# Kernel tuning notes

Hardware: AMD Instinct MI355X
Metric: run time of the kernel (lower is better)

Reference implementation:

```python
import jax, jax.numpy as jnp
import numpy as np

D_MODEL = 1024
N_HEADS = 16
CHUNK_LEN = 50
MEM_LEN = 16
TOTAL_PROB = 20000
TOTAL_SKILL = 1000
B = 64
L = 2000
EPS = 1e-5


def _layernorm(x, g, b):
    mu = jnp.mean(x, axis=-1, keepdims=True)
    var = jnp.var(x, axis=-1, keepdims=True)
    return (x - mu) * jax.lax.rsqrt(var + EPS) * g + b


def setup_inputs() -> dict:
    key = jax.random.key(0)
    ks = jax.random.split(key, 20)
    s = 0.02
    D = D_MODEL
    emb_problem = (jax.random.normal(ks[0], (TOTAL_PROB, D), jnp.float32) * s).at[0].set(0.0)  # padding_idx=0
    emb_skill = (jax.random.normal(ks[1], (TOTAL_SKILL, D), jnp.float32) * s).at[0].set(0.0)
    mem_init = jax.random.normal(ks[2], (1, MEM_LEN, D), jnp.float32) * s
    pos_emb = jax.random.normal(ks[3], (MEM_LEN + CHUNK_LEN, D), jnp.float32) * s
    w_qkv = jax.random.normal(ks[4], (3 * D, D), jnp.float32) * s
    b_qkv = jnp.zeros((3 * D,), jnp.float32)
    w_out = jax.random.normal(ks[5], (D, D), jnp.float32) * s
    b_out = jnp.zeros((D,), jnp.float32)
    w1 = jax.random.normal(ks[6], (4 * D, D), jnp.float32) * s
    b1 = jnp.zeros((4 * D,), jnp.float32)
    w2 = jax.random.normal(ks[7], (D, 4 * D), jnp.float32) * s
    b2 = jnp.zeros((D,), jnp.float32)
    g_attn = jnp.ones((D,), jnp.float32)
    be_attn = jnp.zeros((D,), jnp.float32)
    g_ffn = jnp.ones((D,), jnp.float32)
    be_ffn = jnp.zeros((D,), jnp.float32)
    w_gate = jax.random.normal(ks[8], (D, D), jnp.float32) * s
    b_gate = jnp.zeros((D,), jnp.float32)
    in_prob = jax.random.randint(ks[9], (B, L), 0, TOTAL_PROB, dtype=jnp.int64 if jax.config.jax_enable_x64 else jnp.int32)
    in_skill = jax.random.randint(ks[10], (B, L), 0, TOTAL_SKILL, dtype=jnp.int64 if jax.config.jax_enable_x64 else jnp.int32)
    return dict(in_prob=in_prob, in_skill=in_skill, emb_problem=emb_problem, emb_skill=emb_skill,
                mem_init=mem_init, pos_emb=pos_emb, w_qkv=w_qkv, b_qkv=b_qkv, w_out=w_out, b_out=b_out,
                w1=w1, b1=b1, w2=w2, b2=b2, g_attn=g_attn, be_attn=be_attn, g_ffn=g_ffn, be_ffn=be_ffn,
                w_gate=w_gate, b_gate=b_gate)


def _mha(z, w_qkv, b_qkv, w_out, b_out, mask):
    # z: [B, T, D]; mask: [T, T] bool, True = disallowed (torch attn_mask semantics)
    Bz, T, D = z.shape
    dh = D // N_HEADS
    qkv = z @ w_qkv.T + b_qkv  # [B, T, 3D]
    q, k, v = jnp.split(qkv, 3, axis=-1)
    def heads(x):
        return x.reshape(Bz, T, N_HEADS, dh).transpose(0, 2, 1, 3)  # [B, H, T, dh]
    q, k, v = heads(q), heads(k), heads(v)
    scores = jnp.einsum('bhqd,bhkd->bhqk', q, k) / jnp.sqrt(jnp.float32(dh))
    scores = jnp.where(mask[None, None], jnp.float32(-1e9), scores)
    a = jax.nn.softmax(scores, axis=-1)
    o = jnp.einsum('bhqk,bhkd->bhqd', a, v)  # [B, H, T, dh]
    o = o.transpose(0, 2, 1, 3).reshape(Bz, T, D)
    return o @ w_out.T + b_out


def reference(in_prob, in_skill, emb_problem, emb_skill, mem_init, pos_emb,
              w_qkv, b_qkv, w_out, b_out, w1, b1, w2, b2,
              g_attn, be_attn, g_ffn, be_ffn, w_gate, b_gate):
    Bx, Lx = in_prob.shape
    D = emb_problem.shape[1]
    x = emb_problem[in_prob] + emb_skill[in_skill]  # [B, L, D]
    n_chunks = Lx // CHUNK_LEN
    T = MEM_LEN + CHUNK_LEN
    # block mask: memory fully visible, chunk part strictly causal
    causal = jnp.triu(jnp.ones((CHUNK_LEN, CHUNK_LEN), bool), k=1)
    mask = jnp.zeros((T, T), bool).at[MEM_LEN:, MEM_LEN:].set(causal)
    pos = pos_emb[:T][None]  # [1, T, D]
    chunks = x.reshape(Bx, n_chunks, CHUNK_LEN, D).transpose(1, 0, 2, 3)  # [K, B, Lc, D]
    mem0 = jnp.broadcast_to(mem_init, (Bx, MEM_LEN, D))

    def step(mem, xs):
        chunk, kidx = xs
        z = jnp.concatenate([mem, chunk], axis=1) + pos  # [B, T, D]
        z = z + _mha(_layernorm(z, g_attn, be_attn), w_qkv, b_qkv, w_out, b_out, mask)
        h = _layernorm(z, g_ffn, be_ffn)
        z = z + (jax.nn.relu(h @ w1.T + b1) @ w2.T + b2)
        mem_cand = z[:, :MEM_LEN]
        h_k = z[:, MEM_LEN:]
        g = jax.nn.sigmoid(mem_cand @ w_gate.T + b_gate)
        mem_gated = g * mem_cand + (1.0 - g) * mem
        mem_new = jnp.where(kidx == 0, mem_cand, mem_gated)  # first chunk: no gate
        return mem_new, h_k

    mem_final, hs = jax.lax.scan(step, mem0, (chunks, jnp.arange(n_chunks)))
    enc_out = hs.transpose(1, 0, 2, 3).reshape(Bx, Lx, D)
    return enc_out, mem_final
```

## Files before the change

kernel.cpp:

```cpp
#include <hip/hip_runtime.h>
#include <hip/hip_bf16.h>

#define D_MODEL 1024
#define N_HEADS 16
#define DH 64
#define CHUNK_LEN 50
#define MEM_LEN 16
#define TT 66
#define BB 64
#define LL 2000
#define NCHUNK 40
#define MTOK (BB*TT)

typedef _Float16 half8_t __attribute__((ext_vector_type(8)));
typedef __attribute__((ext_vector_type(4))) float f32x4;

typedef __attribute__((address_space(1))) const void GVoid;
typedef __attribute__((address_space(3))) void LVoid;

__device__ __forceinline__ void gload16(const void* g, void* l) {
  __builtin_amdgcn_global_load_lds((GVoid*)g, (LVoid*)l, 16, 0, 0);
}

__global__ __launch_bounds__(256) void f2h_kernel(const float* __restrict__ in,
                                                  _Float16* __restrict__ out, int n) {
  int i = (blockIdx.x * 256 + threadIdx.x) * 4;
  if (i < n) {
    float4 v = *(const float4*)(in + i);
    out[i+0] = (_Float16)v.x;
    out[i+1] = (_Float16)v.y;
    out[i+2] = (_Float16)v.z;
    out[i+3] = (_Float16)v.w;
  }
}

__global__ __launch_bounds__(256) void build_z_ln(
    const int* __restrict__ in_prob, const int* __restrict__ in_skill,
    const float* __restrict__ emb_p, const float* __restrict__ emb_s,
    const float* __restrict__ mem_src, int mem_bstride,
    const float* __restrict__ pos,
    const float* __restrict__ gam, const float* __restrict__ bet,
    float* __restrict__ z, _Float16* __restrict__ zn, int chunk)
{
  int row = blockIdx.x;
  int b = row / TT, t = row % TT;
  int tid = threadIdx.x;
  int d = tid * 4;
  float4 v;
  if (t < MEM_LEN) {
    v = *(const float4*)(mem_src + (size_t)b*mem_bstride + t*D_MODEL + d);
  } else {
    int tok = chunk*CHUNK_LEN + (t - MEM_LEN);
    int p = in_prob[b*LL + tok];
    int s = in_skill[b*LL + tok];
    float4 vp = *(const float4*)(emb_p + (size_t)p*D_MODEL + d);
    float4 vs = *(const float4*)(emb_s + (size_t)s*D_MODEL + d);
    v = make_float4(vp.x+vs.x, vp.y+vs.y, vp.z+vs.z, vp.w+vs.w);
  }
  float4 pv = *(const float4*)(pos + t*D_MODEL + d);
  v.x += pv.x; v.y += pv.y; v.z += pv.z; v.w += pv.w;
  *(float4*)(z + (size_t)row*D_MODEL + d) = v;
  float sum = v.x+v.y+v.z+v.w;
  float sq  = v.x*v.x+v.y*v.y+v.z*v.z+v.w*v.w;
  #pragma unroll
  for (int off = 32; off; off >>= 1) {
    sum += __shfl_down(sum, off, 64);
    sq  += __shfl_down(sq,  off, 64);
  }
  __shared__ float rs_[4], rq_[4];
  int wave = tid >> 6, lane = tid & 63;
  if (lane == 0) { rs_[wave] = sum; rq_[wave] = sq; }
  __syncthreads();
  sum = rs_[0]+rs_[1]+rs_[2]+rs_[3];
  sq  = rq_[0]+rq_[1]+rq_[2]+rq_[3];
  float mu  = sum * (1.0f/D_MODEL);
  float var = sq  * (1.0f/D_MODEL) - mu*mu;
  float rstd = rsqrtf(var + 1e-5f);
  float4 gv = *(const float4*)(gam + d);
  float4 bv = *(const float4*)(bet + d);
  _Float16* o = zn + (size_t)row*D_MODEL + d;
  o[0] = (_Float16)((v.x-mu)*rstd*gv.x + bv.x);
  o[1] = (_Float16)((v.y-mu)*rstd*gv.y + bv.y);
  o[2] = (_Float16)((v.z-mu)*rstd*gv.z + bv.z);
  o[3] = (_Float16)((v.w-mu)*rstd*gv.w + bv.w);
}

__global__ __launch_bounds__(256) void ln_kernel(
    const float* __restrict__ z, const float* __restrict__ gam, const float* __restrict__ bet,
    _Float16* __restrict__ out)
{
  int row = blockIdx.x;
  int tid = threadIdx.x;
  int d = tid * 4;
  float4 v = *(const float4*)(z + (size_t)row*D_MODEL + d);
  float sum = v.x+v.y+v.z+v.w;
  float sq  = v.x*v.x+v.y*v.y+v.z*v.z+v.w*v.w;
  #pragma unroll
  for (int off = 32; off; off >>= 1) {
    sum += __shfl_down(sum, off, 64);
    sq  += __shfl_down(sq,  off, 64);
  }
  __shared__ float rs_[4], rq_[4];
  int wave = tid >> 6, lane = tid & 63;
  if (lane == 0) { rs_[wave] = sum; rq_[wave] = sq; }
  __syncthreads();
  sum = rs_[0]+rs_[1]+rs_[2]+rs_[3];
  sq  = rq_[0]+rq_[1]+rq_[2]+rq_[3];
  float mu  = sum * (1.0f/D_MODEL);
  float var = sq  * (1.0f/D_MODEL) - mu*mu;
  float rstd = rsqrtf(var + 1e-5f);
  float4 gv = *(const float4*)(gam + d);
  float4 bv = *(const float4*)(bet + d);
  _Float16* o = out + (size_t)row*D_MODEL + d;
  o[0] = (_Float16)((v.x-mu)*rstd*gv.x + bv.x);
  o[1] = (_Float16)((v.y-mu)*rstd*gv.y + bv.y);
  o[2] = (_Float16)((v.z-mu)*rstd*gv.z + bv.z);
  o[3] = (_Float16)((v.w-mu)*rstd*gv.w + bv.w);
}

__global__ __launch_bounds__(256) void attn_kernel(
    const _Float16* __restrict__ qkv, _Float16* __restrict__ attn_o)
{
  __shared__ float qs_t[64*68 + 8];
  __shared__ float ks_t[64*68 + 8];
  __shared__ float vs[TT*DH];
  __shared__ float sc[TT*67];
  int bh = blockIdx.x; int b = bh >> 4, h = bh & 15;
  int tid = threadIdx.x;
  const _Float16* base = qkv + (size_t)b*TT*3072 + h*DH;
  for (int i = tid; i < TT*DH; i += 256) {
    int t = i >> 6, d2 = i & 63;
    const _Float16* rp = base + (size_t)t*3072 + d2;
    qs_t[d2*68 + t] = (float)rp[0];
    ks_t[d2*68 + t] = (float)rp[1024];
    vs[t*64 + d2]   = (float)rp[2048];
  }
  __syncthreads();
  if (tid < 153) {
    int ti = tid / 9, tj = tid % 9;
    int qi0 = ti*4, kj0 = tj*8;
    float acc[4][8];
    #pragma unroll
    for (int i = 0; i < 4; i++)
      #pragma unroll
      for (int j = 0; j < 8; j++) acc[i][j] = 0.f;
    for (int d2 = 0; d2 < 64; d2++) {
      float4 qv = *(const float4*)(qs_t + d2*68 + qi0);
      float4 k0 = *(const float4*)(ks_t + d2*68 + kj0);
      float4 k1 = *(const float4*)(ks_t + d2*68 + kj0 + 4);
      float q_[4] = {qv.x, qv.y, qv.z, qv.w};
      float k_[8] = {k0.x, k0.y, k0.z, k0.w, k1.x, k1.y, k1.z, k1.w};
      #pragma unroll
      for (int i = 0; i < 4; i++)
        #pragma unroll
        for (int j = 0; j < 8; j++)
          acc[i][j] += q_[i]*k_[j];
    }
    #pragma unroll
    for (int i = 0; i < 4; i++) {
      int qi = qi0 + i;
      if (qi >= TT) continue;
      #pragma unroll
      for (int j = 0; j < 8; j++) {
        int kj = kj0 + j;
        if (kj >= TT) continue;
        float s;
        if (qi >= MEM_LEN && kj >= MEM_LEN && kj > qi) s = -1e9f;
        else s = acc[i][j]*0.125f;
        sc[qi*67 + kj] = s;
      }
    }
  }
  __syncthreads();
  if (tid < TT) {
    float* r = sc + tid*67;
    float m = -1e30f;
    for (int j = 0; j < TT; j++) m = fmaxf(m, r[j]);
    float ssum = 0.f;
    for (int j = 0; j < TT; j++) { float e = __expf(r[j]-m); r[j] = e; ssum += e; }
    float inv = 1.f/ssum;
    for (int j = 0; j < TT; j++) r[j] *= inv;
  }
  __syncthreads();
  if (tid < 136) {
    int ti = tid >> 3, tj = tid & 7;
    int qi0 = ti*4, d20 = tj*8;
    float acc[4][8];
    #pragma unroll
    for (int i = 0; i < 4; i++)
      #pragma unroll
      for (int j = 0; j < 8; j++) acc[i][j] = 0.f;
    for (int kj = 0; kj < TT; kj++) {
      float a_[4];
      #pragma unroll
      for (int i = 0; i < 4; i++)
        a_[i] = (qi0 + i < TT) ? sc[(qi0+i)*67 + kj] : 0.f;
      float4 v0 = *(const float4*)(vs + kj*64 + d20);
      float4 v1 = *(const float4*)(vs + kj*64 + d20 + 4);
      float v_[8] = {v0.x, v0.y, v0.z, v0.w, v1.x, v1.y, v1.z, v1.w};
      #pragma unroll
      for (int i = 0; i < 4; i++)
        #pragma unroll
        for (int j = 0; j < 8; j++)
          acc[i][j] += a_[i]*v_[j];
    }
    #pragma unroll
    for (int i = 0; i < 4; i++) {
      int qi = qi0 + i;
      if (qi >= TT) continue;
      _Float16* o = attn_o + ((size_t)b*TT + qi)*D_MODEL + h*DH + d20;
      #pragma unroll
      for (int j = 0; j < 8; j++) o[j] = (_Float16)acc[i][j];
    }
  }
}

__global__ __launch_bounds__(256) void finalize_reduce(
    const float* __restrict__ z, const float* __restrict__ p0, const float* __restrict__ p1,
    const float* __restrict__ b2,
    float* __restrict__ enc_out, float* __restrict__ mem,
    _Float16* __restrict__ mcb, float* __restrict__ mcf, int chunk)
{
  int row = blockIdx.x; int b = row / TT, t = row % TT;
  int d = threadIdx.x * 4;
  size_t idx = (size_t)row*D_MODEL + d;
  float4 v  = *(const float4*)(z  + idx);
  float4 a0 = *(const float4*)(p0 + idx);
  float4 a1 = *(const float4*)(p1 + idx);
  float4 bv = *(const float4*)(b2 + d);
  v.x += a0.x + a1.x + bv.x;
  v.y += a0.y + a1.y + bv.y;
  v.z += a0.z + a1.z + bv.z;
  v.w += a0.w + a1.w + bv.w;
  if (t >= MEM_LEN) {
    size_t o = ((size_t)b*LL + chunk*CHUNK_LEN + (t - MEM_LEN))*D_MODEL + d;
    *(float4*)(enc_out + o) = v;
  } else {
    size_t mrow = (size_t)b*MEM_LEN + t;
    if (chunk == 0) {
      *(float4*)(mem + mrow*D_MODEL + d) = v;
    } else {
      *(float4*)(mcf + mrow*D_MODEL + d) = v;
      _Float16* o = mcb + mrow*D_MODEL + d;
      o[0] = (_Float16)v.x;
      o[1] = (_Float16)v.y;
      o[2] = (_Float16)v.z;
      o[3] = (_Float16)v.w;
    }
  }
}

__global__ __launch_bounds__(256) void copy_mem_kernel(const float* __restrict__ mem,
                                                       float* __restrict__ out) {
  int i = (blockIdx.x * 256 + threadIdx.x) * 4;
  float4 v = *(const float4*)(mem + i);
  *(float4*)(out + i) = v;
}

#define EPI_QKV   0
#define EPI_RESID 1
#define EPI_RELU  2
#define EPI_PART  3

#define KSLICE 2048

template<int EPI>
__global__ __launch_bounds__(256) void gemm_bt(
    const _Float16* __restrict__ A,
    const _Float16* __restrict__ Bw,
    const float* __restrict__ bias,
    float* __restrict__ zres,
    _Float16* __restrict__ obf,
    float* __restrict__ p1,
    int K, int lda, int ldo)
{
  __shared__ short As[2][128*32];
  __shared__ short Bs[2][128*32];
  int tid = threadIdx.x;
  int lane = tid & 63, wave = tid >> 6;
  int wr = wave >> 1, wc = wave & 1;
  int tm = blockIdx.y * 128, tn = blockIdx.x * 128;
  f32x4 acc[4][4] = {};
  const short* Ash = (const short*)A;
  const short* Bsh = (const short*)Bw;
  if constexpr (EPI == EPI_PART) {
    Ash += (size_t)blockIdx.z * KSLICE;
    Bsh += (size_t)blockIdx.z * KSLICE;
  }
  int e0 = tid * 8;
  int r0 = e0 >> 5, c0 = e0 & 31;
  int c0s = c0 ^ (((r0 >> 1) & 3) << 3);
  int ko = (lane >> 4) * 8;
  int rr = lane & 15;
  int swz = ((rr >> 1) & 3) << 3;

  auto STAGE = [&](int buf, int kt) {
    gload16(Ash + (size_t)(tm +      r0)*lda + kt + c0s, (char*)&As[buf][0] +        wave*1024);
    gload16(Ash + (size_t)(tm + 64 + r0)*lda + kt + c0s, (char*)&As[buf][0] + 4096 + wave*1024);
    gload16(Bsh + (size_t)(tn +      r0)*lda + kt + c0s, (char*)&Bs[buf][0] +        wave*1024);
    gload16(Bsh + (size_t)(tn + 64 + r0)*lda + kt + c0s, (char*)&Bs[buf][0] + 4096 + wave*1024);
  };
  auto COMPUTE = [&](int buf) {
    half8_t af[4], bfr[4];
    int kos = ko ^ swz;
    #pragma unroll
    for (int m = 0; m < 4; m++)
      af[m] = *(const half8_t*)(&As[buf][(wr*64 + m*16 + rr)*32 + kos]);
    #pragma unroll
    for (int n = 0; n < 4; n++)
      bfr[n] = *(const half8_t*)(&Bs[buf][(wc*64 + n*16 + rr)*32 + kos]);
    #pragma unroll
    for (int m = 0; m < 4; m++)
      #pragma unroll
      for (int n = 0; n < 4; n++)
        acc[m][n] = __builtin_amdgcn_mfma_f32_16x16x32_f16(af[m], bfr[n], acc[m][n], 0, 0, 0);
  };

  STAGE(0, 0);
  int cur = 0;
  for (int kt = 32; kt < K; kt += 32) {
    STAGE(cur ^ 1, kt);
    asm volatile("s_waitcnt vmcnt(4)" ::: "memory");
    __builtin_amdgcn_s_barrier();
    COMPUTE(cur);
    asm volatile("" ::: "memory");
    __builtin_amdgcn_s_barrier();
    cur ^= 1;
  }
  asm volatile("s_waitcnt vmcnt(0)" ::: "memory");
  __builtin_amdgcn_s_barrier();
  COMPUTE(cur);

  int rbase = tm + wr*64 + ((lane >> 4) << 2);
  int cbase = tn + wc*64 + (lane & 15);
  float* pp = nullptr;
  if constexpr (EPI == EPI_PART) pp = (blockIdx.z == 0) ? zres : p1;
  #pragma unroll
  for (int n = 0; n < 4; n++) {
    int col = cbase + n*16;
    float bs = (EPI == EPI_PART) ? 0.f : bias[col];
    #pragma unroll
    for (int m = 0; m < 4; m++) {
      #pragma unroll
      for (int i = 0; i < 4; i++) {
        int r = rbase + m*16 + i;
        float v = acc[m][n][i] + bs;
        if constexpr (EPI == EPI_QKV) {
          obf[(size_t)r*ldo + col] = (_Float16)v;
        } else if constexpr (EPI == EPI_RESID) {
          zres[(size_t)r*D_MODEL + col] += v;
        } else if constexpr (EPI == EPI_RELU) {
          obf[(size_t)r*ldo + col] = (_Float16)fmaxf(v, 0.f);
        } else {
          pp[(size_t)r*D_MODEL + col] = v;
        }
      }
    }
  }
}

__global__ __launch_bounds__(256) void gemm_gate64(
    const _Float16* __restrict__ A,
    const _Float16* __restrict__ Bw,
    const float* __restrict__ bias,
    const float* __restrict__ mcf,
    float* __restrict__ mem)
{
  __shared__ short As[64*32];
  __shared__ short Bs[64*32];
  int tid = threadIdx.x;
  int lane = tid & 63, wave = tid >> 6;
  int wr = wave >> 1, wc = wave & 1;
  int tm = blockIdx.y * 64, tn = blockIdx.x * 64;
  f32x4 acc[2][2] = {};
  const short* Ash = (const short*)A;
  const short* Bsh = (const short*)Bw;
  int e0 = tid * 8;
  int r0 = e0 >> 5, c0 = e0 & 31;

  for (int kt = 0; kt < 1024; kt += 32) {
    gload16(Ash + (size_t)(tm + r0)*1024 + kt + c0, (char*)As + wave*1024);
    gload16(Bsh + (size_t)(tn + r0)*1024 + kt + c0, (char*)Bs + wave*1024);
    __syncthreads();
    half8_t af[2], bfr[2];
    int ko = (lane >> 4) * 8;
    int rr = lane & 15;
    #pragma unroll
    for (int m = 0; m < 2; m++)
      af[m] = *(const half8_t*)(As + (wr*32 + m*16 + rr)*32 + ko);
    #pragma unroll
    for (int n = 0; n < 2; n++)
      bfr[n] = *(const half8_t*)(Bs + (wc*32 + n*16 + rr)*32 + ko);
    #pragma unroll
    for (int m = 0; m < 2; m++)
      #pragma unroll
      for (int n = 0; n < 2; n++)
        acc[m][n] = __builtin_amdgcn_mfma_f32_16x16x32_f16(af[m], bfr[n], acc[m][n], 0, 0, 0);
    __syncthreads();
  }

  int rbase = tm + wr*32 + ((lane >> 4) << 2);
  int cbase = tn + wc*32 + (lane & 15);
  #pragma unroll
  for (int n = 0; n < 2; n++) {
    int col = cbase + n*16;
    float bs = bias[col];
    #pragma unroll
    for (int m = 0; m < 2; m++) {
      #pragma unroll
      for (int i = 0; i < 4; i++) {
        int r = rbase + m*16 + i;
        float g = 1.f / (1.f + __expf(-(acc[m][n][i] + bs)));
        size_t mi = (size_t)r*D_MODEL + col;
        mem[mi] = g*mcf[mi] + (1.f - g)*mem[mi];
      }
    }
  }
}

extern "C" void kernel_launch(void* const* d_in, const int* in_sizes, int n_in,
                              void* d_out, int out_size, void* d_ws, size_t ws_size,
                              hipStream_t stream) {
  const int*   in_prob  = (const int*)d_in[0];
  const int*   in_skill = (const int*)d_in[1];
  const float* emb_p    = (const float*)d_in[2];
  const float* emb_s    = (const float*)d_in[3];
  const float* mem_init = (const float*)d_in[4];
  const float* pos      = (const float*)d_in[5];
  const float* w_qkv    = (const float*)d_in[6];
  const float* b_qkv    = (const float*)d_in[7];
  const float* w_out    = (const float*)d_in[8];
  const float* b_out    = (const float*)d_in[9];
  const float* w1       = (const float*)d_in[10];
  const float* b1       = (const float*)d_in[11];
  const float* w2       = (const float*)d_in[12];
  const float* b2       = (const float*)d_in[13];
  const float* g_attn   = (const float*)d_in[14];
  const float* be_attn  = (const float*)d_in[15];
  const float* g_ffn    = (const float*)d_in[16];
  const float* be_ffn   = (const float*)d_in[17];
  const float* w_gate   = (const float*)d_in[18];
  const float* b_gate   = (const float*)d_in[19];

  float* enc_out = (float*)d_out;
  float* mem_out = enc_out + (size_t)BB*LL*D_MODEL;

  char* ws = (char*)d_ws;
  size_t off = 0;
  auto alloc = [&](size_t bytes) -> char* {
    char* p = ws + off;
    off += (bytes + 255) & ~(size_t)255;
    return p;
  };
  _Float16* wqkv_h = (_Float16*)alloc((size_t)3072*1024*2);
  _Float16* wout_h = (_Float16*)alloc((size_t)1024*1024*2);
  _Float16* w1_h   = (_Float16*)alloc((size_t)4096*1024*2);
  _Float16* w2_h   = (_Float16*)alloc((size_t)1024*4096*2);
  _Float16* wgate_h= (_Float16*)alloc((size_t)1024*1024*2);
  float*    z      = (float*)alloc((size_t)MTOK*D_MODEL*4);
  _Float16* zn     = (_Float16*)alloc((size_t)MTOK*D_MODEL*2);
  _Float16* qkv    = (_Float16*)alloc((size_t)MTOK*3072*2);
  _Float16* ao     = (_Float16*)alloc((size_t)MTOK*D_MODEL*2);
  _Float16* hb     = (_Float16*)alloc((size_t)MTOK*D_MODEL*2);
  _Float16* fh     = (_Float16*)alloc((size_t)MTOK*4096*2);
  _Float16* mcb    = (_Float16*)alloc((size_t)1024*1024*2);
  float*    mem    = (float*)alloc((size_t)1024*1024*4);
  float*    mcf    = (float*)alloc((size_t)1024*1024*4);
  float*    part0  = (float*)alloc((size_t)MTOK*D_MODEL*4);
  float*    part1  = (float*)alloc((size_t)MTOK*D_MODEL*4);
  if (off > ws_size) return;

  f2h_kernel<<<(3072*1024)/1024, 256, 0, stream>>>(w_qkv, wqkv_h, 3072*1024);
  f2h_kernel<<<(1024*1024)/1024, 256, 0, stream>>>(w_out, wout_h, 1024*1024);
  f2h_kernel<<<(4096*1024)/1024, 256, 0, stream>>>(w1, w1_h, 4096*1024);
  f2h_kernel<<<(1024*4096)/1024, 256, 0, stream>>>(w2, w2_h, 1024*4096);
  f2h_kernel<<<(1024*1024)/1024, 256, 0, stream>>>(w_gate, wgate_h, 1024*1024);

  for (int c = 0; c < NCHUNK; c++) {
    const float* msrc = (c == 0) ? mem_init : mem;
    int mbs = (c == 0) ? 0 : MEM_LEN*D_MODEL;
    build_z_ln<<<MTOK, 256, 0, stream>>>(in_prob, in_skill, emb_p, emb_s,
                                         msrc, mbs, pos, g_attn, be_attn, z, zn, c);
    gemm_bt<EPI_QKV><<<dim3(3072/128, MTOK/128), 256, 0, stream>>>(
        zn, wqkv_h, b_qkv, nullptr, qkv, nullptr, 1024, 1024, 3072);
    attn_kernel<<<BB*N_HEADS, 256, 0, stream>>>(qkv, ao);
    gemm_bt<EPI_RESID><<<dim3(1024/128, MTOK/128), 256, 0, stream>>>(
        ao, wout_h, b_out, z, nullptr, nullptr, 1024, 1024, 1024);
    ln_kernel<<<MTOK, 256, 0, stream>>>(z, g_ffn, be_ffn, hb);
    gemm_bt<EPI_RELU><<<dim3(4096/128, MTOK/128), 256, 0, stream>>>(
        hb, w1_h, b1, nullptr, fh, nullptr, 1024, 1024, 4096);
    gemm_bt<EPI_PART><<<dim3(1024/128, MTOK/128, 2), 256, 0, stream>>>(
        fh, w2_h, b2, part0, nullptr, part1, KSLICE, 4096, 1024);
    finalize_reduce<<<MTOK, 256, 0, stream>>>(z, part0, part1, b2,
                                              enc_out, mem, mcb, mcf, c);
    if (c > 0) {
      gemm_gate64<<<dim3(1024/64, 1024/64), 256, 0, stream>>>(
          mcb, wgate_h, b_gate, mcf, mem);
    }
  }
  copy_mem_kernel<<<(1024*1024)/1024, 256, 0, stream>>>(mem, mem_out);
}
```

Measured before the change: 11.55 ms.

## Fuse FFN output reduction into w2 GEMM epilogue and drop split-K

Removes the two-way split-K on the second FFN GEMM and the separate finalize_reduce kernel. The GEMM epilogue now adds the residual and bias and scatters results directly to enc_out, memory, or the gate candidate buffers. This removes partial-sum writes and reads plus one launch. It halves the grid of that GEMM and doubles its K loop, which risks poor CU occupancy and a tail wave.

```diff
diff --git a/kernel.cpp b/kernel.cpp
--- a/kernel.cpp
+++ b/kernel.cpp
@@ -11,6 +11,7 @@
 #define LL 2000
 #define NCHUNK 40
 #define MTOK (BB*TT)
+#define MROW (BB*MEM_LEN)
 
 typedef _Float16 half8_t __attribute__((ext_vector_type(8)));
 typedef __attribute__((ext_vector_type(4))) float f32x4;
@@ -215,41 +216,6 @@
   }
 }
 
-__global__ __launch_bounds__(256) void finalize_reduce(
-    const float* __restrict__ z, const float* __restrict__ p0, const float* __restrict__ p1,
-    const float* __restrict__ b2,
-    float* __restrict__ enc_out, float* __restrict__ mem,
-    _Float16* __restrict__ mcb, float* __restrict__ mcf, int chunk)
-{
-  int row = blockIdx.x; int b = row / TT, t = row % TT;
-  int d = threadIdx.x * 4;
-  size_t idx = (size_t)row*D_MODEL + d;
-  float4 v  = *(const float4*)(z  + idx);
-  float4 a0 = *(const float4*)(p0 + idx);
-  float4 a1 = *(const float4*)(p1 + idx);
-  float4 bv = *(const float4*)(b2 + d);
-  v.x += a0.x + a1.x + bv.x;
-  v.y += a0.y + a1.y + bv.y;
-  v.z += a0.z + a1.z + bv.z;
-  v.w += a0.w + a1.w + bv.w;
-  if (t >= MEM_LEN) {
-    size_t o = ((size_t)b*LL + chunk*CHUNK_LEN + (t - MEM_LEN))*D_MODEL + d;
-    *(float4*)(enc_out + o) = v;
-  } else {
-    size_t mrow = (size_t)b*MEM_LEN + t;
-    if (chunk == 0) {
-      *(float4*)(mem + mrow*D_MODEL + d) = v;
-    } else {
-      *(float4*)(mcf + mrow*D_MODEL + d) = v;
-      _Float16* o = mcb + mrow*D_MODEL + d;
-      o[0] = (_Float16)v.x;
-      o[1] = (_Float16)v.y;
-      o[2] = (_Float16)v.z;
-      o[3] = (_Float16)v.w;
-    }
-  }
-}
-
 __global__ __launch_bounds__(256) void copy_mem_kernel(const float* __restrict__ mem,
                                                        float* __restrict__ out) {
   int i = (blockIdx.x * 256 + threadIdx.x) * 4;
@@ -260,9 +226,7 @@
 #define EPI_QKV   0
 #define EPI_RESID 1
 #define EPI_RELU  2
-#define EPI_PART  3
-
-#define KSLICE 2048
+#define EPI_FIN   3
 
 template<int EPI>
 __global__ __launch_bounds__(256) void gemm_bt(
@@ -271,8 +235,10 @@
     const float* __restrict__ bias,
     float* __restrict__ zres,
     _Float16* __restrict__ obf,
-    float* __restrict__ p1,
-    int K, int lda, int ldo)
+    float* __restrict__ enc,
+    float* __restrict__ memp,
+    float* __restrict__ mcfp,
+    int chunk, int K, int lda, int ldo)
 {
   __shared__ short As[2][128*32];
   __shared__ short Bs[2][128*32];
@@ -283,16 +249,12 @@
   f32x4 acc[4][4] = {};
   const short* Ash = (const short*)A;
   const short* Bsh = (const short*)Bw;
-  if constexpr (EPI == EPI_PART) {
-    Ash += (size_t)blockIdx.z * KSLICE;
-    Bsh += (size_t)blockIdx.z * KSLICE;
-  }
   int e0 = tid * 8;
   int r0 = e0 >> 5, c0 = e0 & 31;
   int c0s = c0 ^ (((r0 >> 1) & 3) << 3);
   int ko = (lane >> 4) * 8;
   int rr = lane & 15;
-  int swz = ((rr >> 1) & 3) << 3;
+  int kos = ko ^ (((rr >> 1) & 3) << 3);
 
   auto STAGE = [&](int buf, int kt) {
     gload16(Ash + (size_t)(tm +      r0)*lda + kt + c0s, (char*)&As[buf][0] +        wave*1024);
@@ -302,7 +264,6 @@
   };
   auto COMPUTE = [&](int buf) {
     half8_t af[4], bfr[4];
-    int kos = ko ^ swz;
     #pragma unroll
     for (int m = 0; m < 4; m++)
       af[m] = *(const half8_t*)(&As[buf][(wr*64 + m*16 + rr)*32 + kos]);
@@ -333,18 +294,16 @@
 
   int rbase = tm + wr*64 + ((lane >> 4) << 2);
   int cbase = tn + wc*64 + (lane & 15);
-  float* pp = nullptr;
-  if constexpr (EPI == EPI_PART) pp = (blockIdx.z == 0) ? zres : p1;
   #pragma unroll
-  for (int n = 0; n < 4; n++) {
-    int col = cbase + n*16;
-    float bs = (EPI == EPI_PART) ? 0.f : bias[col];
+  for (int nn = 0; nn < 4; nn++) {
+    int col = cbase + nn*16;
+    float bs = bias[col];
     #pragma unroll
     for (int m = 0; m < 4; m++) {
       #pragma unroll
       for (int i = 0; i < 4; i++) {
         int r = rbase + m*16 + i;
-        float v = acc[m][n][i] + bs;
+        float v = acc[m][nn][i] + bs;
         if constexpr (EPI == EPI_QKV) {
           obf[(size_t)r*ldo + col] = (_Float16)v;
         } else if constexpr (EPI == EPI_RESID) {
@@ -352,7 +311,19 @@
         } else if constexpr (EPI == EPI_RELU) {
           obf[(size_t)r*ldo + col] = (_Float16)fmaxf(v, 0.f);
         } else {
-          pp[(size_t)r*D_MODEL + col] = v;
+          float vfin = zres[(size_t)r*D_MODEL + col] + v;
+          int b = r / TT, t = r % TT;
+          if (t >= MEM_LEN) {
+            enc[((size_t)b*LL + (size_t)chunk*CHUNK_LEN + (t - MEM_LEN))*D_MODEL + col] = vfin;
+          } else {
+            size_t mi = ((size_t)b*MEM_LEN + t)*D_MODEL + col;
+            if (chunk == 0) {
+              memp[mi] = vfin;
+            } else {
+              mcfp[mi] = vfin;
+              obf[mi] = (_Float16)vfin;
+            }
+          }
         }
       }
     }
@@ -463,11 +434,9 @@
   _Float16* ao     = (_Float16*)alloc((size_t)MTOK*D_MODEL*2);
   _Float16* hb     = (_Float16*)alloc((size_t)MTOK*D_MODEL*2);
   _Float16* fh     = (_Float16*)alloc((size_t)MTOK*4096*2);
-  _Float16* mcb    = (_Float16*)alloc((size_t)1024*1024*2);
-  float*    mem    = (float*)alloc((size_t)1024*1024*4);
-  float*    mcf    = (float*)alloc((size_t)1024*1024*4);
-  float*    part0  = (float*)alloc((size_t)MTOK*D_MODEL*4);
-  float*    part1  = (float*)alloc((size_t)MTOK*D_MODEL*4);
+  _Float16* mcb    = (_Float16*)alloc((size_t)MROW*D_MODEL*2);
+  float*    mem    = (float*)alloc((size_t)MROW*D_MODEL*4);
+  float*    mcf    = (float*)alloc((size_t)MROW*D_MODEL*4);
   if (off > ws_size) return;
 
   f2h_kernel<<<(3072*1024)/1024, 256, 0, stream>>>(w_qkv, wqkv_h, 3072*1024);
@@ -482,21 +451,19 @@
     build_z_ln<<<MTOK, 256, 0, stream>>>(in_prob, in_skill, emb_p, emb_s,
                                          msrc, mbs, pos, g_attn, be_attn, z, zn, c);
     gemm_bt<EPI_QKV><<<dim3(3072/128, MTOK/128), 256, 0, stream>>>(
-        zn, wqkv_h, b_qkv, nullptr, qkv, nullptr, 1024, 1024, 3072);
+        zn, wqkv_h, b_qkv, nullptr, qkv, nullptr, nullptr, nullptr, 0, 1024, 1024, 3072);
     attn_kernel<<<BB*N_HEADS, 256, 0, stream>>>(qkv, ao);
     gemm_bt<EPI_RESID><<<dim3(1024/128, MTOK/128), 256, 0, stream>>>(
-        ao, wout_h, b_out, z, nullptr, nullptr, 1024, 1024, 1024);
+        ao, wout_h, b_out, z, nullptr, nullptr, nullptr, nullptr, 0, 1024, 1024, 1024);
     ln_kernel<<<MTOK, 256, 0, stream>>>(z, g_ffn, be_ffn, hb);
     gemm_bt<EPI_RELU><<<dim3(4096/128, MTOK/128), 256, 0, stream>>>(
-        hb, w1_h, b1, nullptr, fh, nullptr, 1024, 1024, 4096);
-    gemm_bt<EPI_PART><<<dim3(1024/128, MTOK/128, 2), 256, 0, stream>>>(
-        fh, w2_h, b2, part0, nullptr, part1, KSLICE, 4096, 1024);
-    finalize_reduce<<<MTOK, 256, 0, stream>>>(z, part0, part1, b2,
-                                              enc_out, mem, mcb, mcf, c);
+        hb, w1_h, b1, nullptr, fh, nullptr, nullptr, nullptr, 0, 1024, 1024, 4096);
+    gemm_bt<EPI_FIN><<<dim3(1024/128, MTOK/128), 256, 0, stream>>>(
+        fh, w2_h, b2, z, mcb, enc_out, mem, mcf, c, 4096, 4096, 1024);
     if (c > 0) {
       gemm_gate64<<<dim3(1024/64, 1024/64), 256, 0, stream>>>(
           mcb, wgate_h, b_gate, mcf, mem);
     }
   }
-  copy_mem_kernel<<<(1024*1024)/1024, 256, 0, stream>>>(mem, mem_out);
-}
+  copy_mem_kernel<<<(MROW*D_MODEL)/1024, 256, 0, stream>>>(mem, mem_out);
+}
```

New measurement: 12.53 ms. 8.5% more time.

## Split recurrent memory path from chunk-token FFN and batch tail work across all chunks

Applied to the files above, without the earlier changes.

Inside the 40-step recurrence, only the memory rows (16 per batch) feed the next step. This change runs the out-projection, FFN and finalize for those rows alone inside the loop, and stores chunk-token attention outputs as fp16 in the output buffer. Afterwards it runs the out-projection, LN, FFN and residual for all 128k chunk tokens as large batched GEMM groups, processed in reverse order so the fp16 staging area is not overwritten before it is read. The goal is to take most GEMM work off the serial critical path and give it larger, better-occupied launches. The cost is extra workspace sizing logic and a fallback path, and correctness depends on the aliasing order inside d_out.

```diff
diff --git a/kernel.cpp b/kernel.cpp
--- a/kernel.cpp
+++ b/kernel.cpp
@@ -11,6 +11,8 @@
 #define LL 2000
 #define NCHUNK 40
 #define MTOK (BB*TT)
+#define MROW (BB*MEM_LEN)
+#define MALLR ((size_t)BB*LL)
 
 typedef _Float16 half8_t __attribute__((ext_vector_type(8)));
 typedef __attribute__((ext_vector_type(4))) float f32x4;
@@ -32,6 +34,33 @@
     out[i+2] = (_Float16)v.z;
     out[i+3] = (_Float16)v.w;
   }
+}
+
+__device__ __forceinline__ void ln_row(float4 v, int tid, int d,
+                                       const float* gam, const float* bet,
+                                       _Float16* o) {
+  float sum = v.x+v.y+v.z+v.w;
+  float sq  = v.x*v.x+v.y*v.y+v.z*v.z+v.w*v.w;
+  #pragma unroll
+  for (int off = 32; off; off >>= 1) {
+    sum += __shfl_down(sum, off, 64);
+    sq  += __shfl_down(sq,  off, 64);
+  }
+  __shared__ float rs_[4], rq_[4];
+  int wave = tid >> 6, lane = tid & 63;
+  if (lane == 0) { rs_[wave] = sum; rq_[wave] = sq; }
+  __syncthreads();
+  sum = rs_[0]+rs_[1]+rs_[2]+rs_[3];
+  sq  = rq_[0]+rq_[1]+rq_[2]+rq_[3];
+  float mu  = sum * (1.0f/D_MODEL);
+  float var = sq  * (1.0f/D_MODEL) - mu*mu;
+  float rstd = rsqrtf(var + 1e-5f);
+  float4 gv = *(const float4*)(gam + d);
+  float4 bv = *(const float4*)(bet + d);
+  o[0] = (_Float16)((v.x-mu)*rstd*gv.x + bv.x);
+  o[1] = (_Float16)((v.y-mu)*rstd*gv.y + bv.y);
+  o[2] = (_Float16)((v.z-mu)*rstd*gv.z + bv.z);
+  o[3] = (_Float16)((v.w-mu)*rstd*gv.w + bv.w);
 }
 
 __global__ __launch_bounds__(256) void build_z_ln(
@@ -60,29 +89,59 @@
   float4 pv = *(const float4*)(pos + t*D_MODEL + d);
   v.x += pv.x; v.y += pv.y; v.z += pv.z; v.w += pv.w;
   *(float4*)(z + (size_t)row*D_MODEL + d) = v;
-  float sum = v.x+v.y+v.z+v.w;
-  float sq  = v.x*v.x+v.y*v.y+v.z*v.z+v.w*v.w;
-  #pragma unroll
-  for (int off = 32; off; off >>= 1) {
-    sum += __shfl_down(sum, off, 64);
-    sq  += __shfl_down(sq,  off, 64);
-  }
-  __shared__ float rs_[4], rq_[4];
-  int wave = tid >> 6, lane = tid & 63;
-  if (lane == 0) { rs_[wave] = sum; rq_[wave] = sq; }
-  __syncthreads();
-  sum = rs_[0]+rs_[1]+rs_[2]+rs_[3];
-  sq  = rq_[0]+rq_[1]+rq_[2]+rq_[3];
-  float mu  = sum * (1.0f/D_MODEL);
-  float var = sq  * (1.0f/D_MODEL) - mu*mu;
-  float rstd = rsqrtf(var + 1e-5f);
-  float4 gv = *(const float4*)(gam + d);
-  float4 bv = *(const float4*)(bet + d);
-  _Float16* o = zn + (size_t)row*D_MODEL + d;
-  o[0] = (_Float16)((v.x-mu)*rstd*gv.x + bv.x);
-  o[1] = (_Float16)((v.y-mu)*rstd*gv.y + bv.y);
-  o[2] = (_Float16)((v.z-mu)*rstd*gv.z + bv.z);
-  o[3] = (_Float16)((v.w-mu)*rstd*gv.w + bv.w);
+  ln_row(v, tid, d, gam, bet, zn + (size_t)row*D_MODEL + d);
+}
+
+__global__ __launch_bounds__(256) void build_z_ln_lite(
+    const int* __restrict__ in_prob, const int* __restrict__ in_skill,
+    const float* __restrict__ emb_p, const float* __restrict__ emb_s,
+    const float* __restrict__ mem_src, int mem_bstride,
+    const float* __restrict__ pos,
+    const float* __restrict__ gam, const float* __restrict__ bet,
+    float* __restrict__ z_mem, _Float16* __restrict__ zn, int chunk)
+{
+  int row = blockIdx.x;
+  int b = row / TT, t = row % TT;
+  int tid = threadIdx.x;
+  int d = tid * 4;
+  float4 v;
+  if (t < MEM_LEN) {
+    v = *(const float4*)(mem_src + (size_t)b*mem_bstride + t*D_MODEL + d);
+  } else {
+    int tok = chunk*CHUNK_LEN + (t - MEM_LEN);
+    int p = in_prob[b*LL + tok];
+    int s = in_skill[b*LL + tok];
+    float4 vp = *(const float4*)(emb_p + (size_t)p*D_MODEL + d);
+    float4 vs = *(const float4*)(emb_s + (size_t)s*D_MODEL + d);
+    v = make_float4(vp.x+vs.x, vp.y+vs.y, vp.z+vs.z, vp.w+vs.w);
+  }
+  float4 pv = *(const float4*)(pos + t*D_MODEL + d);
+  v.x += pv.x; v.y += pv.y; v.z += pv.z; v.w += pv.w;
+  if (t < MEM_LEN)
+    *(float4*)(z_mem + ((size_t)b*MEM_LEN + t)*D_MODEL + d) = v;
+  ln_row(v, tid, d, gam, bet, zn + (size_t)row*D_MODEL + d);
+}
+
+__global__ __launch_bounds__(256) void build_zbase_group(
+    const int* __restrict__ in_prob, const int* __restrict__ in_skill,
+    const float* __restrict__ emb_p, const float* __restrict__ emb_s,
+    const float* __restrict__ pos,
+    float* __restrict__ zf, size_t r0)
+{
+  size_t rg = r0 + blockIdx.x;
+  int b = (int)(rg / LL);
+  int tok = (int)(rg - (size_t)b*LL);
+  int t = MEM_LEN + (tok % CHUNK_LEN);
+  int tid = threadIdx.x;
+  int d = tid * 4;
+  int p = in_prob[rg];
+  int s = in_skill[rg];
+  float4 vp = *(const float4*)(emb_p + (size_t)p*D_MODEL + d);
+  float4 vs = *(const float4*)(emb_s + (size_t)s*D_MODEL + d);
+  float4 v = make_float4(vp.x+vs.x, vp.y+vs.y, vp.z+vs.z, vp.w+vs.w);
+  float4 pv = *(const float4*)(pos + t*D_MODEL + d);
+  v.x += pv.x; v.y += pv.y; v.z += pv.z; v.w += pv.w;
+  *(float4*)(zf + (size_t)blockIdx.x*D_MODEL + d) = v;
 }
 
 __global__ __launch_bounds__(256) void ln_kernel(
@@ -93,41 +152,12 @@
   int tid = threadIdx.x;
   int d = tid * 4;
   float4 v = *(const float4*)(z + (size_t)row*D_MODEL + d);
-  float sum = v.x+v.y+v.z+v.w;
-  float sq  = v.x*v.x+v.y*v.y+v.z*v.z+v.w*v.w;
-  #pragma unroll
-  for (int off = 32; off; off >>= 1) {
-    sum += __shfl_down(sum, off, 64);
-    sq  += __shfl_down(sq,  off, 64);
-  }
-  __shared__ float rs_[4], rq_[4];
-  int wave = tid >> 6, lane = tid & 63;
-  if (lane == 0) { rs_[wave] = sum; rq_[wave] = sq; }
-  __syncthreads();
-  sum = rs_[0]+rs_[1]+rs_[2]+rs_[3];
-  sq  = rq_[0]+rq_[1]+rq_[2]+rq_[3];
-  float mu  = sum * (1.0f/D_MODEL);
-  float var = sq  * (1.0f/D_MODEL) - mu*mu;
-  float rstd = rsqrtf(var + 1e-5f);
-  float4 gv = *(const float4*)(gam + d);
-  float4 bv = *(const float4*)(bet + d);
-  _Float16* o = out + (size_t)row*D_MODEL + d;
-  o[0] = (_Float16)((v.x-mu)*rstd*gv.x + bv.x);
-  o[1] = (_Float16)((v.y-mu)*rstd*gv.y + bv.y);
-  o[2] = (_Float16)((v.z-mu)*rstd*gv.z + bv.z);
-  o[3] = (_Float16)((v.w-mu)*rstd*gv.w + bv.w);
-}
-
-__global__ __launch_bounds__(256) void attn_kernel(
-    const _Float16* __restrict__ qkv, _Float16* __restrict__ attn_o)
-{
-  __shared__ float qs_t[64*68 + 8];
-  __shared__ float ks_t[64*68 + 8];
-  __shared__ float vs[TT*DH];
-  __shared__ float sc[TT*67];
-  int bh = blockIdx.x; int b = bh >> 4, h = bh & 15;
-  int tid = threadIdx.x;
-  const _Float16* base = qkv + (size_t)b*TT*3072 + h*DH;
+  ln_row(v, tid, d, gam, bet, out + (size_t)row*D_MODEL + d);
+}
+
+__device__ __forceinline__ void attn_core(
+    const _Float16* base, float* qs_t, float* ks_t, float* vs, float* sc, int tid)
+{
   for (int i = tid; i < TT*DH; i += 256) {
     int t = i >> 6, d2 = i & 63;
     const _Float16* rp = base + (size_t)t*3072 + d2;
@@ -182,6 +212,18 @@
     for (int j = 0; j < TT; j++) r[j] *= inv;
   }
   __syncthreads();
+}
+
+__global__ __launch_bounds__(256) void attn_kernel(
+    const _Float16* __restrict__ qkv, _Float16* __restrict__ attn_o)
+{
+  __shared__ float qs_t[64*68 + 8];
+  __shared__ float ks_t[64*68 + 8];
+  __shared__ float vs[TT*DH];
+  __shared__ float sc[TT*67];
+  int bh = blockIdx.x; int b = bh >> 4, h = bh & 15;
+  int tid = threadIdx.x;
+  attn_core(qkv + (size_t)b*TT*3072 + h*DH, qs_t, ks_t, vs, sc, tid);
   if (tid < 136) {
     int ti = tid >> 3, tj = tid & 7;
     int qi0 = ti*4, d20 = tj*8;
@@ -209,6 +251,56 @@
       int qi = qi0 + i;
       if (qi >= TT) continue;
       _Float16* o = attn_o + ((size_t)b*TT + qi)*D_MODEL + h*DH + d20;
+      #pragma unroll
+      for (int j = 0; j < 8; j++) o[j] = (_Float16)acc[i][j];
+    }
+  }
+}
+
+__global__ __launch_bounds__(256) void attn_split(
+    const _Float16* __restrict__ qkv,
+    _Float16* __restrict__ aoM, _Float16* __restrict__ ao16, int chunk)
+{
+  __shared__ float qs_t[64*68 + 8];
+  __shared__ float ks_t[64*68 + 8];
+  __shared__ float vs[TT*DH];
+  __shared__ float sc[TT*67];
+  int bh = blockIdx.x; int b = bh >> 4, h = bh & 15;
+  int tid = threadIdx.x;
+  attn_core(qkv + (size_t)b*TT*3072 + h*DH, qs_t, ks_t, vs, sc, tid);
+  if (tid < 136) {
+    int ti = tid >> 3, tj = tid & 7;
+    int qi0 = ti*4, d20 = tj*8;
+    float acc[4][8];
+    #pragma unroll
+    for (int i = 0; i < 4; i++)
+      #pragma unroll
+      for (int j = 0; j < 8; j++) acc[i][j] = 0.f;
+    for (int kj = 0; kj < TT; kj++) {
+      float a_[4];
+      #pragma unroll
+      for (int i = 0; i < 4; i++)
+        a_[i] = (qi0 + i < TT) ? sc[(qi0+i)*67 + kj] : 0.f;
+      float4 v0 = *(const float4*)(vs + kj*64 + d20);
+      float4 v1 = *(const float4*)(vs + kj*64 + d20 + 4);
+      float v_[8] = {v0.x, v0.y, v0.z, v0.w, v1.x, v1.y, v1.z, v1.w};
+      #pragma unroll
+      for (int i = 0; i < 4; i++)
+        #pragma unroll
+        for (int j = 0; j < 8; j++)
+          acc[i][j] += a_[i]*v_[j];
+    }
+    #pragma unroll
+    for (int i = 0; i < 4; i++) {
+      int qi = qi0 + i;
+      if (qi >= TT) continue;
+      _Float16* o;
+      if (qi < MEM_LEN) {
+        o = aoM + ((size_t)b*MEM_LEN + qi)*D_MODEL + h*DH + d20;
+      } else {
+        size_t rg = (size_t)b*LL + (size_t)chunk*CHUNK_LEN + (qi - MEM_LEN);
+        o = ao16 + rg*D_MODEL + h*DH + d20;
+      }
       #pragma unroll
       for (int j = 0; j < 8; j++) o[j] = (_Float16)acc[i][j];
     }
@@ -233,7 +325,7 @@
   v.z += a0.z + a1.z + bv.z;
   v.w += a0.w + a1.w + bv.w;
   if (t >= MEM_LEN) {
-    size_t o = ((size_t)b*LL + chunk*CHUNK_LEN + (t - MEM_LEN))*D_MODEL + d;
+    size_t o = ((size_t)b*LL + (size_t)chunk*CHUNK_LEN + (t - MEM_LEN))*D_MODEL + d;
     *(float4*)(enc_out + o) = v;
   } else {
     size_t mrow = (size_t)b*MEM_LEN + t;
@@ -242,12 +334,52 @@
     } else {
       *(float4*)(mcf + mrow*D_MODEL + d) = v;
       _Float16* o = mcb + mrow*D_MODEL + d;
-      o[0] = (_Float16)v.x;
-      o[1] = (_Float16)v.y;
-      o[2] = (_Float16)v.z;
-      o[3] = (_Float16)v.w;
-    }
-  }
+      o[0] = (_Float16)v.x; o[1] = (_Float16)v.y; o[2] = (_Float16)v.z; o[3] = (_Float16)v.w;
+    }
+  }
+}
+
+__global__ __launch_bounds__(256) void finalize_mem(
+    const float* __restrict__ z, const float* __restrict__ p0, const float* __restrict__ p1,
+    const float* __restrict__ b2,
+    float* __restrict__ mem, _Float16* __restrict__ mcb, float* __restrict__ mcf, int chunk)
+{
+  int row = blockIdx.x;
+  int d = threadIdx.x * 4;
+  size_t idx = (size_t)row*D_MODEL + d;
+  float4 v  = *(const float4*)(z  + idx);
+  float4 a0 = *(const float4*)(p0 + idx);
+  float4 a1 = *(const float4*)(p1 + idx);
+  float4 bv = *(const float4*)(b2 + d);
+  v.x += a0.x + a1.x + bv.x;
+  v.y += a0.y + a1.y + bv.y;
+  v.z += a0.z + a1.z + bv.z;
+  v.w += a0.w + a1.w + bv.w;
+  if (chunk == 0) {
+    *(float4*)(mem + idx) = v;
+  } else {
+    *(float4*)(mcf + idx) = v;
+    _Float16* o = mcb + idx;
+    o[0] = (_Float16)v.x; o[1] = (_Float16)v.y; o[2] = (_Float16)v.z; o[3] = (_Float16)v.w;
+  }
+}
+
+__global__ __launch_bounds__(256) void finalize_enc(
+    const float* __restrict__ zf, const float* __restrict__ p0, const float* __restrict__ p1,
+    const float* __restrict__ b2, float* __restrict__ enc, size_t r0)
+{
+  size_t row = blockIdx.x;
+  int d = threadIdx.x * 4;
+  size_t idx = row*D_MODEL + d;
+  float4 v  = *(const float4*)(zf + idx);
+  float4 a0 = *(const float4*)(p0 + idx);
+  float4 a1 = *(const float4*)(p1 + idx);
+  float4 bv = *(const float4*)(b2 + d);
+  v.x += a0.x + a1.x + bv.x;
+  v.y += a0.y + a1.y + bv.y;
+  v.z += a0.z + a1.z + bv.z;
+  v.w += a0.w + a1.w + bv.w;
+  *(float4*)(enc + (r0 + row)*D_MODEL + d) = v;
 }
 
 __global__ __launch_bounds__(256) void copy_mem_kernel(const float* __restrict__ mem,
@@ -292,7 +424,7 @@
   int c0s = c0 ^ (((r0 >> 1) & 3) << 3);
   int ko = (lane >> 4) * 8;
   int rr = lane & 15;
-  int swz = ((rr >> 1) & 3) << 3;
+  int kos = ko ^ (((rr >> 1) & 3) << 3);
 
   auto STAGE = [&](int buf, int kt) {
     gload16(Ash + (size_t)(tm +      r0)*lda + kt + c0s, (char*)&As[buf][0] +        wave*1024);
@@ -302,7 +434,6 @@
   };
   auto COMPUTE = [&](int buf) {
     half8_t af[4], bfr[4];
-    int kos = ko ^ swz;
     #pragma unroll
     for (int m = 0; m < 4; m++)
       af[m] = *(const half8_t*)(&As[buf][(wr*64 + m*16 + rr)*32 + kos]);
@@ -336,15 +467,15 @@
   float* pp = nullptr;
   if constexpr (EPI == EPI_PART) pp = (blockIdx.z == 0) ? zres : p1;
   #pragma unroll
-  for (int n = 0; n < 4; n++) {
-    int col = cbase + n*16;
+  for (int nn = 0; nn < 4; nn++) {
+    int col = cbase + nn*16;
     float bs = (EPI == EPI_PART) ? 0.f : bias[col];
     #pragma unroll
     for (int m = 0; m < 4; m++) {
       #pragma unroll
       for (int i = 0; i < 4; i++) {
         int r = rbase + m*16 + i;
-        float v = acc[m][n][i] + bs;
+        float v = acc[m][nn][i] + bs;
         if constexpr (EPI == EPI_QKV) {
           obf[(size_t)r*ldo + col] = (_Float16)v;
         } else if constexpr (EPI == EPI_RESID) {
@@ -443,7 +574,8 @@
   const float* b_gate   = (const float*)d_in[19];
 
   float* enc_out = (float*)d_out;
-  float* mem_out = enc_out + (size_t)BB*LL*D_MODEL;
+  float* mem_out = enc_out + MALLR*D_MODEL;
+  _Float16* ao16 = (_Float16*)d_out;
 
   char* ws = (char*)d_ws;
   size_t off = 0;
@@ -457,18 +589,36 @@
   _Float16* w1_h   = (_Float16*)alloc((size_t)4096*1024*2);
   _Float16* w2_h   = (_Float16*)alloc((size_t)1024*4096*2);
   _Float16* wgate_h= (_Float16*)alloc((size_t)1024*1024*2);
-  float*    z      = (float*)alloc((size_t)MTOK*D_MODEL*4);
   _Float16* zn     = (_Float16*)alloc((size_t)MTOK*D_MODEL*2);
   _Float16* qkv    = (_Float16*)alloc((size_t)MTOK*3072*2);
-  _Float16* ao     = (_Float16*)alloc((size_t)MTOK*D_MODEL*2);
-  _Float16* hb     = (_Float16*)alloc((size_t)MTOK*D_MODEL*2);
-  _Float16* fh     = (_Float16*)alloc((size_t)MTOK*4096*2);
-  _Float16* mcb    = (_Float16*)alloc((size_t)1024*1024*2);
-  float*    mem    = (float*)alloc((size_t)1024*1024*4);
-  float*    mcf    = (float*)alloc((size_t)1024*1024*4);
-  float*    part0  = (float*)alloc((size_t)MTOK*D_MODEL*4);
-  float*    part1  = (float*)alloc((size_t)MTOK*D_MODEL*4);
-  if (off > ws_size) return;
+  _Float16* mcb    = (_Float16*)alloc((size_t)MROW*D_MODEL*2);
+  float*    mem    = (float*)alloc((size_t)MROW*D_MODEL*4);
+  float*    mcf    = (float*)alloc((size_t)MROW*D_MODEL*4);
+  size_t union_base = off;
+
+  auto rnd = [](size_t b) { return (b + 255) & ~(size_t)255; };
+  const size_t tm_fixed =
+      rnd((size_t)MROW*D_MODEL*4) +
+      rnd((size_t)MROW*D_MODEL*2) +
+      rnd((size_t)MROW*D_MODEL*2) +
+      rnd((size_t)MROW*4096*2) +
+      rnd((size_t)MROW*D_MODEL*4) +
+      rnd((size_t)MROW*D_MODEL*4);
+  auto gr_bytes = [&](size_t GR) {
+    return rnd(GR*D_MODEL*4) + rnd(GR*D_MODEL*2) + rnd(GR*4096*2)
+         + rnd(GR*D_MODEL*4) + rnd(GR*D_MODEL*4);
+  };
+  const size_t fb_bytes =
+      rnd((size_t)MTOK*D_MODEL*4) + rnd((size_t)MTOK*D_MODEL*2) +
+      rnd((size_t)MTOK*D_MODEL*2) + rnd((size_t)MTOK*4096*2) +
+      rnd((size_t)MTOK*D_MODEL*4) + rnd((size_t)MTOK*D_MODEL*4);
+  size_t GR = 0;
+  const size_t cand[3] = {16000, 6400, 3200};
+  for (int i = 0; i < 3; i++) {
+    if (union_base + tm_fixed + gr_bytes(cand[i]) <= ws_size) { GR = cand[i]; break; }
+  }
+  bool tailmode = (GR != 0);
+  if (!tailmode && union_base + fb_bytes > ws_size) return;
 
   f2h_kernel<<<(3072*1024)/1024, 256, 0, stream>>>(w_qkv, wqkv_h, 3072*1024);
   f2h_kernel<<<(1024*1024)/1024, 256, 0, stream>>>(w_out, wout_h, 1024*1024);
@@ -476,27 +626,84 @@
   f2h_kernel<<<(1024*4096)/1024, 256, 0, stream>>>(w2, w2_h, 1024*4096);
   f2h_kernel<<<(1024*1024)/1024, 256, 0, stream>>>(w_gate, wgate_h, 1024*1024);
 
-  for (int c = 0; c < NCHUNK; c++) {
-    const float* msrc = (c == 0) ? mem_init : mem;
-    int mbs = (c == 0) ? 0 : MEM_LEN*D_MODEL;
-    build_z_ln<<<MTOK, 256, 0, stream>>>(in_prob, in_skill, emb_p, emb_s,
-                                         msrc, mbs, pos, g_attn, be_attn, z, zn, c);
-    gemm_bt<EPI_QKV><<<dim3(3072/128, MTOK/128), 256, 0, stream>>>(
-        zn, wqkv_h, b_qkv, nullptr, qkv, nullptr, 1024, 1024, 3072);
-    attn_kernel<<<BB*N_HEADS, 256, 0, stream>>>(qkv, ao);
-    gemm_bt<EPI_RESID><<<dim3(1024/128, MTOK/128), 256, 0, stream>>>(
-        ao, wout_h, b_out, z, nullptr, nullptr, 1024, 1024, 1024);
-    ln_kernel<<<MTOK, 256, 0, stream>>>(z, g_ffn, be_ffn, hb);
-    gemm_bt<EPI_RELU><<<dim3(4096/128, MTOK/128), 256, 0, stream>>>(
-        hb, w1_h, b1, nullptr, fh, nullptr, 1024, 1024, 4096);
-    gemm_bt<EPI_PART><<<dim3(1024/128, MTOK/128, 2), 256, 0, stream>>>(
-        fh, w2_h, b2, part0, nullptr, part1, KSLICE, 4096, 1024);
-    finalize_reduce<<<MTOK, 256, 0, stream>>>(z, part0, part1, b2,
-                                              enc_out, mem, mcb, mcf, c);
-    if (c > 0) {
-      gemm_gate64<<<dim3(1024/64, 1024/64), 256, 0, stream>>>(
-          mcb, wgate_h, b_gate, mcf, mem);
-    }
-  }
-  copy_mem_kernel<<<(1024*1024)/1024, 256, 0, stream>>>(mem, mem_out);
-}
+  if (tailmode) {
+    float*    z_mem = (float*)alloc((size_t)MROW*D_MODEL*4);
+    _Float16* ao_m  = (_Float16*)alloc((size_t)MROW*D_MODEL*2);
+    _Float16* hb_m  = (_Float16*)alloc((size_t)MROW*D_MODEL*2);
+    _Float16* fh_m  = (_Float16*)alloc((size_t)MROW*4096*2);
+    float*    p0m   = (float*)alloc((size_t)MROW*D_MODEL*4);
+    float*    p1m   = (float*)alloc((size_t)MROW*D_MODEL*4);
+    float*    zf    = (float*)alloc(GR*D_MODEL*4);
+    _Float16* hbR   = (_Float16*)alloc(GR*D_MODEL*2);
+    _Float16* fhR   = (_Float16*)alloc(GR*4096*2);
+    float*    p0R   = (float*)alloc(GR*D_MODEL*4);
+    float*    p1R   = (float*)alloc(GR*D_MODEL*4);
+
+    for (int c = 0; c < NCHUNK; c++) {
+      const float* msrc = (c == 0) ? mem_init : mem;
+      int mbs = (c == 0) ? 0 : MEM_LEN*D_MODEL;
+      build_z_ln_lite<<<MTOK, 256, 0, stream>>>(in_prob, in_skill, emb_p, emb_s,
+                                                msrc, mbs, pos, g_attn, be_attn, z_mem, zn, c);
+      gemm_bt<EPI_QKV><<<dim3(3072/128, MTOK/128), 256, 0, stream>>>(
+          zn, wqkv_h, b_qkv, nullptr, qkv, nullptr, 1024, 1024, 3072);
+      attn_split<<<BB*N_HEADS, 256, 0, stream>>>(qkv, ao_m, ao16, c);
+      gemm_bt<EPI_RESID><<<dim3(1024/128, MROW/128), 256, 0, stream>>>(
+          ao_m, wout_h, b_out, z_mem, nullptr, nullptr, 1024, 1024, 1024);
+      ln_kernel<<<MROW, 256, 0, stream>>>(z_mem, g_ffn, be_ffn, hb_m);
+      gemm_bt<EPI_RELU><<<dim3(4096/128, MROW/128), 256, 0, stream>>>(
+          hb_m, w1_h, b1, nullptr, fh_m, nullptr, 1024, 1024, 4096);
+      gemm_bt<EPI_PART><<<dim3(1024/128, MROW/128, 2), 256, 0, stream>>>(
+          fh_m, w2_h, nullptr, p0m, nullptr, p1m, KSLICE, 4096, 1024);
+      finalize_mem<<<MROW, 256, 0, stream>>>(z_mem, p0m, p1m, b2, mem, mcb, mcf, c);
+      if (c > 0) {
+        gemm_gate64<<<dim3(1024/64, 1024/64), 256, 0, stream>>>(
+            mcb, wgate_h, b_gate, mcf, mem);
+      }
+    }
+
+    int ngroups = (int)(MALLR / GR);
+    for (int g = ngroups - 1; g >= 0; --g) {
+      size_t r0 = (size_t)g * GR;
+      build_zbase_group<<<(int)GR, 256, 0, stream>>>(in_prob, in_skill, emb_p, emb_s,
+                                                     pos, zf, r0);
+      gemm_bt<EPI_RESID><<<dim3(1024/128, (int)(GR/128)), 256, 0, stream>>>(
+          ao16 + r0*D_MODEL, wout_h, b_out, zf, nullptr, nullptr, 1024, 1024, 1024);
+      ln_kernel<<<(int)GR, 256, 0, stream>>>(zf, g_ffn, be_ffn, hbR);
+      gemm_bt<EPI_RELU><<<dim3(4096/128, (int)(GR/128)), 256, 0, stream>>>(
+          hbR, w1_h, b1, nullptr, fhR, nullptr, 1024, 1024, 4096);
+      gemm_bt<EPI_PART><<<dim3(1024/128, (int)(GR/128), 2), 256, 0, stream>>>(
+          fhR, w2_h, nullptr, p0R, nullptr, p1R, KSLICE, 4096, 1024);
+      finalize_enc<<<(int)GR, 256, 0, stream>>>(zf, p0R, p1R, b2, enc_out, r0);
+    }
+  } else {
+    float*    z   = (float*)alloc((size_t)MTOK*D_MODEL*4);
+    _Float16* ao  = (_Float16*)alloc((size_t)MTOK*D_MODEL*2);
+    _Float16* hb  = (_Float16*)alloc((size_t)MTOK*D_MODEL*2);
+    _Float16* fh  = (_Float16*)alloc((size_t)MTOK*4096*2);
+    float*    p0f = (float*)alloc((size_t)MTOK*D_MODEL*4);
+    float*    p1f = (float*)alloc((size_t)MTOK*D_MODEL*4);
+    for (int c = 0; c < NCHUNK; c++) {
+      const float* msrc = (c == 0) ? mem_init : mem;
+      int mbs = (c == 0) ? 0 : MEM_LEN*D_MODEL;
+      build_z_ln<<<MTOK, 256, 0, stream>>>(in_prob, in_skill, emb_p, emb_s,
+                                           msrc, mbs, pos, g_attn, be_attn, z, zn, c);
+      gemm_bt<EPI_QKV><<<dim3(3072/128, MTOK/128), 256, 0, stream>>>(
+          zn, wqkv_h, b_qkv, nullptr, qkv, nullptr, 1024, 1024, 3072);
+      attn_kernel<<<BB*N_HEADS, 256, 0, stream>>>(qkv, ao);
+      gemm_bt<EPI_RESID><<<dim3(1024/128, MTOK/128), 256, 0, stream>>>(
+          ao, wout_h, b_out, z, nullptr, nullptr, 1024, 1024, 1024);
+      ln_kernel<<<MTOK, 256, 0, stream>>>(z, g_ffn, be_ffn, hb);
+      gemm_bt<EPI_RELU><<<dim3(4096/128, MTOK/128), 256, 0, stream>>>(
+          hb, w1_h, b1, nullptr, fh, nullptr, 1024, 1024, 4096);
+      gemm_bt<EPI_PART><<<dim3(1024/128, MTOK/128, 2), 256, 0, stream>>>(
+          fh, w2_h, nullptr, p0f, nullptr, p1f, KSLICE, 4096, 1024);
+      finalize_reduce<<<MTOK, 256, 0, stream>>>(z, p0f, p1f, b2,
+                                                enc_out, mem, mcb, mcf, c);
+      if (c > 0) {
+        gemm_gate64<<<dim3(1024/64, 1024/64), 256, 0, stream>>>(
+            mcb, wgate_h, b_gate, mcf, mem);
+      }
+    }
+  }
+  copy_mem_kernel<<<(MROW*D_MODEL)/1024, 256, 0, stream>>>(mem, mem_out);
+}
```

Result: slower. 13.10 ms (+13.4%).
